# Performance work log

Hardware: AMD Instinct MI355X
Metric: run time of the kernel (lower is better)

## Reference

```python
import jax, jax.numpy as jnp
import numpy as np

B, T, V, D, SLOTS = 16, 4096, 32000, 512, 256
EPS = 1e-5


def setup_inputs() -> dict:
    key = jax.random.key(0)
    ks = jax.random.split(key, 12)
    s = 0.02
    return {
        "seq": jax.random.randint(ks[0], (B, T), 0, V),
        "emb": jax.random.normal(ks[1], (V, D), jnp.float32) * s,
        "w1": jax.random.normal(ks[2], (D, 2 * D), jnp.float32) * s,
        "b1": jnp.zeros((2 * D,), jnp.float32),
        "w2": jax.random.normal(ks[3], (2 * D, D), jnp.float32) * s,
        "b2": jnp.zeros((D,), jnp.float32),
        "ln_g": jnp.ones((D,), jnp.float32),
        "ln_b": jnp.zeros((D,), jnp.float32),
        "wg": jax.random.normal(ks[4], (D,), jnp.float32) * s,
        "bg": jnp.zeros((), jnp.float32),
        "wq": jax.random.normal(ks[5], (D, D), jnp.float32) * s,
        "bq": jnp.zeros((D,), jnp.float32),
        "wo": jax.random.normal(ks[6], (D, V), jnp.float32) * s,
        "bo": jnp.zeros((V,), jnp.float32),
    }


def reference(seq, emb, w1, b1, w2, b2, ln_g, ln_b, wg, bg, wq, bq, wo, bo):
    # Encoder: embed -> residual FFN -> LayerNorm
    h0 = emb[seq]                                        # [B,T,D]
    ff = jax.nn.relu(h0 @ w1 + b1) @ w2 + b2             # [B,T,D]
    x = h0 + ff
    mu = jnp.mean(x, axis=-1, keepdims=True)
    var = jnp.mean(jnp.square(x - mu), axis=-1, keepdims=True)
    h = (x - mu) * jax.lax.rsqrt(var + EPS) * ln_g + ln_b  # [B,T,D]

    # Gate -> top-k slot selection -> gather memory
    gate = jax.nn.sigmoid(h @ wg + bg)                   # [B,T]
    topk = min(SLOTS, T)
    _, top_idx = jax.lax.top_k(gate, topk)               # [B,K]
    memory = jnp.take_along_axis(h, top_idx[:, :, None], axis=1)  # [B,K,D]

    # Single-query masked softmax attention (mask is all ones)
    query_h = h[:, -1, :]                                # [B,D]
    q = query_h @ wq + bq                                # [B,D]
    scores = jnp.einsum('bkd,bd->bk', memory, q)         # [B,K]
    mask = jnp.ones((seq.shape[0], topk), jnp.float32)
    scores = jnp.where(mask == 0, -1e9, scores)
    attn = jax.nn.softmax(scores, axis=-1)               # [B,K]
    ctx = jnp.einsum('bk,bkd->bd', attn, memory)         # [B,D]
    return ctx @ wo + bo                                 # [B,V]
```

## Files before the change

### kernel.cpp

```cpp
#include <hip/hip_runtime.h>

typedef __bf16 bf16x8 __attribute__((ext_vector_type(8)));
typedef float f32x4 __attribute__((ext_vector_type(4)));
typedef unsigned short ushort8v __attribute__((ext_vector_type(8)));

#define NB 16
#define NT 4096
#define NV 32000
#define ND 512
#define NH 1024
#define NSLOTS 256

__device__ __forceinline__ float b2f(unsigned short u) {
  unsigned int x = ((unsigned int)u) << 16;
  return __builtin_bit_cast(float, x);
}
__device__ __forceinline__ unsigned short f2b(float f) {
  unsigned int x = __builtin_bit_cast(unsigned int, f);
  unsigned int r = (x + 0x7FFFu + ((x >> 16) & 1u)) >> 16;
  return (unsigned short)r;
}

#define GLOAD_LDS16(g, l)                                                              \
  __builtin_amdgcn_global_load_lds((const __attribute__((address_space(1))) void*)(g), \
                                   (__attribute__((address_space(3))) void*)(l), 16, 0, 0)
#define BARRIER() asm volatile("s_barrier" ::: "memory")
#define VMCNT(n) asm volatile("s_waitcnt vmcnt(" #n ")" ::: "memory")

__global__ __launch_bounds__(256) void cvtwt_kernel(
    const float* __restrict__ emb, unsigned short* __restrict__ embb,
    const float* __restrict__ w1, const float* __restrict__ w2,
    unsigned short* __restrict__ w1t, unsigned short* __restrict__ w2t) {
  const int blk = blockIdx.x;
  if (blk < 8000) {
    const long base = ((long)blk * 256 + threadIdx.x) * 8;
    float4 a = *(const float4*)&emb[base];
    float4 b = *(const float4*)&emb[base + 4];
    ushort8v o;
    o[0] = f2b(a.x); o[1] = f2b(a.y); o[2] = f2b(a.z); o[3] = f2b(a.w);
    o[4] = f2b(b.x); o[5] = f2b(b.y); o[6] = f2b(b.z); o[7] = f2b(b.w);
    *(ushort8v*)&embb[base] = o;
  } else {
    const int i = (blk - 8000) * 256 + threadIdx.x;
    if (i < ND * NH) {
      const int n = i >> 9, k = i & 511;
      w1t[i] = f2b(w1[k * NH + n]);
    } else {
      const int j = i - ND * NH;
      const int n = j >> 10, k = j & 1023;
      w2t[j] = f2b(w2[k * ND + n]);
    }
  }
}

template <int KDIM, int NLD, int NBN, bool RELU>
__global__ __launch_bounds__(256) void gemm128_kernel(
    const unsigned short* __restrict__ Abase, const unsigned short* __restrict__ Bt,
    const float* __restrict__ bias, unsigned short* __restrict__ Out) {
  __shared__ union {
    unsigned short AB[3][2][128 * 32];
    unsigned short C[128 * 136];
  } sm;
  const int tid = threadIdx.x;
  const int lane = tid & 63;
  const int w = tid >> 6;

  const int id = blockIdx.x;
  const int swz = (id & 7) * (gridDim.x >> 3) + (id >> 3);
  const int bm = swz / NBN;
  const int bn = swz % NBN;

  const int wm = w >> 1, wn = w & 1;

  const int rgrp = lane >> 2;
  const int schunk = (lane & 3) ^ ((lane >> 3) & 3);
  const unsigned short* aptr[2];
  const unsigned short* bptr[2];
#pragma unroll
  for (int r = 0; r < 2; ++r) {
    const int grp = w * 2 + r;
    const int arow = bm * 128 + grp * 16 + rgrp;
    aptr[r] = Abase + (size_t)arow * (size_t)KDIM + schunk * 8;
    const int brow = bn * 128 + grp * 16 + rgrp;
    bptr[r] = Bt + (size_t)brow * (size_t)KDIM + schunk * 8;
  }

  const int fr = lane & 15;
  const int fhi = lane >> 4;
  const int fsw = (fr >> 1) & 3;
  const int fchunk = (fhi ^ fsw) * 8;
  int aoff[4], boff[4];
#pragma unroll
  for (int m = 0; m < 4; ++m) aoff[m] = (wm * 64 + m * 16 + fr) * 32 + fchunk;
#pragma unroll
  for (int n = 0; n < 4; ++n) boff[n] = (wn * 64 + n * 16 + fr) * 32 + fchunk;

  f32x4 acc[4][4] = {};

  auto stage = [&](int buf, int kt) {
#pragma unroll
    for (int r = 0; r < 2; ++r) {
      const int grp = w * 2 + r;
      GLOAD_LDS16(aptr[r] + kt * 32, &sm.AB[buf][0][grp * 512]);
      GLOAD_LDS16(bptr[r] + kt * 32, &sm.AB[buf][1][grp * 512]);
    }
  };

  constexpr int NKT = KDIM / 32;
  stage(0, 0);
  stage(1, 1);
  for (int kt = 0; kt < NKT; ++kt) {
    if (kt + 1 < NKT)
      asm volatile("s_waitcnt vmcnt(4)" ::: "memory");
    else
      asm volatile("s_waitcnt vmcnt(0)" ::: "memory");
    __builtin_amdgcn_s_barrier();
    if (kt + 2 < NKT) stage((kt + 2) % 3, kt + 2);
    const int cur = kt % 3;
    bf16x8 af[4], bfr[4];
#pragma unroll
    for (int m = 0; m < 4; ++m)
      af[m] = __builtin_bit_cast(bf16x8, *(const ushort8v*)&sm.AB[cur][0][aoff[m]]);
#pragma unroll
    for (int n = 0; n < 4; ++n)
      bfr[n] = __builtin_bit_cast(bf16x8, *(const ushort8v*)&sm.AB[cur][1][boff[n]]);
    __builtin_amdgcn_s_setprio(1);
#pragma unroll
    for (int m = 0; m < 4; ++m)
#pragma unroll
      for (int n = 0; n < 4; ++n)
        acc[m][n] = __builtin_amdgcn_mfma_f32_16x16x32_bf16(af[m], bfr[n], acc[m][n], 0, 0, 0);
    __builtin_amdgcn_s_setprio(0);
  }
  __builtin_amdgcn_s_barrier();

#pragma unroll
  for (int m = 0; m < 4; ++m)
#pragma unroll
    for (int n = 0; n < 4; ++n) {
      const int col_l = wn * 64 + n * 16 + fr;
      const float bb = bias[bn * 128 + col_l];
      const int row_l0 = wm * 64 + m * 16 + (fhi << 2);
#pragma unroll
      for (int i = 0; i < 4; ++i) {
        float v = acc[m][n][i] + bb;
        if constexpr (RELU) v = fmaxf(v, 0.f);
        sm.C[(row_l0 + i) * 136 + col_l] = f2b(v);
      }
    }
  __syncthreads();
#pragma unroll
  for (int r8 = 0; r8 < 8; ++r8) {
    const int chunk = r8 * 256 + tid;
    const int row = chunk >> 4;
    const int c8 = (chunk & 15) * 8;
    ushort8v v = *(const ushort8v*)&sm.C[row * 136 + c8];
    *(ushort8v*)&Out[(size_t)(bm * 128 + row) * (size_t)NLD + bn * 128 + c8] = v;
  }
}

__global__ __launch_bounds__(256) void lnv_kernel(
    const float* __restrict__ emb, const unsigned short* __restrict__ FFv,
    unsigned short* __restrict__ Hv, const float* __restrict__ ln_g,
    const float* __restrict__ ln_b, const float* __restrict__ wg,
    const float* __restrict__ bgp, float* __restrict__ gatev,
    const int* __restrict__ seq, float* __restrict__ hlast) {
  const int lane = threadIdx.x & 63;
  const int w = threadIdx.x >> 6;
  const int v = blockIdx.x * 4 + w;
  const float* er = emb + (size_t)v * ND + lane * 8;
  ushort8v fv = *(const ushort8v*)&FFv[(size_t)v * ND + lane * 8];
  float4 e0 = *(const float4*)er, e1 = *(const float4*)(er + 4);
  float x[8] = {b2f(fv[0]) + e0.x, b2f(fv[1]) + e0.y, b2f(fv[2]) + e0.z, b2f(fv[3]) + e0.w,
                b2f(fv[4]) + e1.x, b2f(fv[5]) + e1.y, b2f(fv[6]) + e1.z, b2f(fv[7]) + e1.w};
  float s = 0.f, sq = 0.f;
#pragma unroll
  for (int j = 0; j < 8; ++j) {
    s += x[j];
    sq += x[j] * x[j];
  }
#pragma unroll
  for (int o = 32; o; o >>= 1) {
    s += __shfl_xor(s, o);
    sq += __shfl_xor(sq, o);
  }
  const float mu = s * (1.f / 512.f);
  const float var = sq * (1.f / 512.f) - mu * mu;
  const float rs = rsqrtf(var + 1e-5f);
  float gd = 0.f;
  float h[8];
  ushort8v hv;
#pragma unroll
  for (int j = 0; j < 8; ++j) {
    const int col = lane * 8 + j;
    h[j] = (x[j] - mu) * rs * ln_g[col] + ln_b[col];
    hv[j] = f2b(h[j]);
    gd += h[j] * wg[col];
  }
  *(ushort8v*)&Hv[(size_t)v * ND + lane * 8] = hv;
#pragma unroll
  for (int o = 32; o; o >>= 1) gd += __shfl_xor(gd, o);
  if (lane == 0) gatev[v] = 1.f / (1.f + expf(-(gd + bgp[0])));
  for (int b = 0; b < NB; ++b) {
    if (seq[b * NT + NT - 1] == v) {
      float* hl = hlast + b * ND + lane * 8;
#pragma unroll
      for (int j = 0; j < 8; ++j) hl[j] = h[j];
    }
  }
}

__global__ __launch_bounds__(256) void topk_qpart_kernel(
    const float* __restrict__ gatev, const int* __restrict__ seq,
    int* __restrict__ topidx, const float* __restrict__ hlast,
    const float* __restrict__ wq, const float* __restrict__ bq,
    float* __restrict__ qpart) {
  __shared__ int wsum[2][4];
  __shared__ unsigned int scanbuf[256];
  const int tid = threadIdx.x;
  if (blockIdx.x >= 16) {
    const int blk = blockIdx.x - 16;
    const int b = blk >> 3, s = blk & 7;
    const int d0 = s * 64;
    float a0 = 0.f, a1 = 0.f;
#pragma unroll 4
    for (int dd = 0; dd < 64; ++dd) {
      const float hv = hlast[b * ND + d0 + dd];
      a0 += hv * wq[(size_t)(d0 + dd) * ND + tid];
      a1 += hv * wq[(size_t)(d0 + dd) * ND + tid + 256];
    }
    if (s == 0) {
      a0 += bq[tid];
      a1 += bq[tid + 256];
    }
    float* qp = qpart + ((size_t)b * 8 + s) * ND;
    qp[tid] = a0;
    qp[tid + 256] = a1;
    return;
  }
  const int b = blockIdx.x;
  const int wv = tid >> 6;
  const int lane = tid & 63;
  const int* sq_ = seq + (size_t)b * NT;
  const int base = tid * 16;
  unsigned int kreg[16];
#pragma unroll
  for (int j = 0; j < 16; ++j)
    kreg[j] = __builtin_bit_cast(unsigned int, gatev[sq_[base + j]]);

  unsigned int K = 0u;
  for (int bit = 31; bit >= 0; --bit) {
    const unsigned int cand = K | (1u << bit);
    int c = 0;
#pragma unroll
    for (int j = 0; j < 16; ++j) c += (kreg[j] >= cand) ? 1 : 0;
#pragma unroll
    for (int o = 32; o; o >>= 1) c += __shfl_xor(c, o);
    const int par = bit & 1;
    if (lane == 0) wsum[par][wv] = c;
    __syncthreads();
    const int tot = wsum[par][0] + wsum[par][1] + wsum[par][2] + wsum[par][3];
    if (tot >= NSLOTS) K = cand;
  }
  int gcnt = 0, ecnt = 0;
#pragma unroll
  for (int j = 0; j < 16; ++j) {
    gcnt += (kreg[j] > K) ? 1 : 0;
    ecnt += (kreg[j] == K) ? 1 : 0;
  }
  __syncthreads();
  scanbuf[tid] = ((unsigned int)gcnt << 16) | (unsigned int)ecnt;
  __syncthreads();
  for (int off = 1; off < 256; off <<= 1) {
    unsigned int v2 = (tid >= off) ? scanbuf[tid - off] : 0u;
    __syncthreads();
    scanbuf[tid] += v2;
    __syncthreads();
  }
  const unsigned int my = scanbuf[tid];
  const unsigned int tot = scanbuf[255];
  const int gi = (int)(my >> 16);
  const int ei = (int)(my & 0xFFFFu);
  const int tot_gt = (int)(tot >> 16);
  int gpos = gi - gcnt;
  int epos = tot_gt + (ei - ecnt);
  int* outp = topidx + b * NSLOTS;
#pragma unroll
  for (int j = 0; j < 16; ++j) {
    if (kreg[j] > K) {
      outp[gpos++] = base + j;
    } else if (kreg[j] == K) {
      if (epos < NSLOTS) outp[epos] = base + j;
      epos++;
    }
  }
}

__global__ __launch_bounds__(256) void attn_kernel(
    const unsigned short* __restrict__ Hv, const int* __restrict__ seq,
    const float* __restrict__ qpart, const int* __restrict__ topidx,
    float* __restrict__ ctx) {
  __shared__ float qs[512];
  __shared__ float attnv[256];
  __shared__ int idxs[256];
  __shared__ float red[4];
  __shared__ float part[2][128];
  const int blk = blockIdx.x;
  const int b = blk >> 2, dc = blk & 3;
  const int tid = threadIdx.x;
  const int lane = tid & 63, wv = tid >> 6;
  {
    float a0 = 0.f, a1 = 0.f;
#pragma unroll
    for (int s = 0; s < 8; ++s) {
      const float* qp = qpart + ((size_t)b * 8 + s) * ND;
      a0 += qp[tid];
      a1 += qp[tid + 256];
    }
    qs[tid] = a0;
    qs[tid + 256] = a1;
  }
  idxs[tid] = seq[(size_t)b * NT + topidx[b * 256 + tid]];
  __syncthreads();
  const unsigned short* hr = Hv + (size_t)idxs[tid] * ND;
  float sc = 0.f;
  for (int d0 = 0; d0 < 512; d0 += 8) {
    ushort8v hv = *(const ushort8v*)&hr[d0];
#pragma unroll
    for (int j = 0; j < 8; ++j) sc += b2f(hv[j]) * qs[d0 + j];
  }
  float m = sc;
#pragma unroll
  for (int o = 32; o; o >>= 1) m = fmaxf(m, __shfl_xor(m, o));
  if (lane == 0) red[wv] = m;
  __syncthreads();
  m = fmaxf(fmaxf(red[0], red[1]), fmaxf(red[2], red[3]));
  __syncthreads();
  const float e = expf(sc - m);
  float ssum = e;
#pragma unroll
  for (int o = 32; o; o >>= 1) ssum += __shfl_xor(ssum, o);
  if (lane == 0) red[wv] = ssum;
  __syncthreads();
  ssum = red[0] + red[1] + red[2] + red[3];
  attnv[tid] = e / ssum;
  __syncthreads();
  const int d = dc * 128 + (tid & 127);
  const int kh = tid >> 7;
  float c = 0.f;
#pragma unroll 4
  for (int k2 = 0; k2 < 128; ++k2) {
    const int k = kh * 128 + k2;
    c += attnv[k] * b2f(Hv[(size_t)idxs[k] * ND + d]);
  }
  part[kh][tid & 127] = c;
  __syncthreads();
  if (tid < 128) ctx[b * 512 + dc * 128 + tid] = part[0][tid] + part[1][tid];
}

__global__ __launch_bounds__(256) void out_part_kernel(const float* __restrict__ ctx,
                                                       const float* __restrict__ wo,
                                                       float* __restrict__ part) {
  const int blk = blockIdx.x;
  const int ct = blk % 125, s = blk / 125;
  const int v = ct * 256 + threadIdx.x;
  const int d0 = s * 64;
  const float* wp = wo + (size_t)d0 * NV + v;
  float acc[16] = {};
#pragma unroll 4
  for (int dd = 0; dd < 64; ++dd) {
    const float wv = wp[(size_t)dd * NV];
#pragma unroll
    for (int bb = 0; bb < 16; ++bb) acc[bb] += ctx[bb * ND + d0 + dd] * wv;
  }
  float* pp = part + (size_t)s * NB * NV + v;
#pragma unroll
  for (int bb = 0; bb < 16; ++bb) pp[(size_t)bb * NV] = acc[bb];
}

__global__ __launch_bounds__(256) void out_reduce_kernel(const float* __restrict__ part,
                                                         const float* __restrict__ bo,
                                                         float* __restrict__ out) {
  const int i = blockIdx.x * 256 + threadIdx.x;
  const int b = i / NV;
  const int v = i - b * NV;
  float a = bo[v];
#pragma unroll
  for (int s = 0; s < 8; ++s) a += part[(size_t)s * NB * NV + i];
  out[i] = a;
}

extern "C" void kernel_launch(void* const* d_in, const int* in_sizes, int n_in,
                              void* d_out, int out_size, void* d_ws, size_t ws_size,
                              hipStream_t stream) {
  const int* seq = (const int*)d_in[0];
  const float* emb = (const float*)d_in[1];
  const float* w1 = (const float*)d_in[2];
  const float* b1 = (const float*)d_in[3];
  const float* w2 = (const float*)d_in[4];
  const float* b2 = (const float*)d_in[5];
  const float* ln_g = (const float*)d_in[6];
  const float* ln_b = (const float*)d_in[7];
  const float* wg = (const float*)d_in[8];
  const float* bg = (const float*)d_in[9];
  const float* wq = (const float*)d_in[10];
  const float* bq = (const float*)d_in[11];
  const float* wo = (const float*)d_in[12];
  const float* bo = (const float*)d_in[13];
  float* out = (float*)d_out;

  char* ws = (char*)d_ws;
  unsigned short* A1v = (unsigned short*)ws;
  unsigned short* FFv = (unsigned short*)(ws + ((size_t)64 << 20));
  unsigned short* embb = (unsigned short*)(ws + ((size_t)96 << 20));
  unsigned short* Hv = (unsigned short*)(ws + ((size_t)128 << 20));
  float* part = (float*)(ws + ((size_t)160 << 20));
  unsigned short* w1t = (unsigned short*)(ws + ((size_t)177 << 20));
  unsigned short* w2t = (unsigned short*)(ws + ((size_t)178 << 20));
  char* sb = ws + ((size_t)180 << 20);
  float* gatev = (float*)sb;
  int* topidx = (int*)(sb + 131072);
  float* hlast = (float*)(sb + 131072 + 16384);
  float* ctxbuf = (float*)(sb + 131072 + 16384 + 32768);
  float* qpart = (float*)(sb + 131072 + 16384 + 65536);

  cvtwt_kernel<<<12096, 256, 0, stream>>>(emb, embb, w1, w2, w1t, w2t);
  gemm128_kernel<512, 1024, 8, true>
      <<<2000, 256, 0, stream>>>(embb, w1t, b1, A1v);
  gemm128_kernel<1024, 512, 4, false>
      <<<1000, 256, 0, stream>>>(A1v, w2t, b2, FFv);
  lnv_kernel<<<8000, 256, 0, stream>>>(emb, FFv, Hv, ln_g, ln_b, wg, bg, gatev, seq, hlast);
  topk_qpart_kernel<<<144, 256, 0, stream>>>(gatev, seq, topidx, hlast, wq, bq, qpart);
  attn_kernel<<<64, 256, 0, stream>>>(Hv, seq, qpart, topidx, ctxbuf);
  out_part_kernel<<<1000, 256, 0, stream>>>(ctxbuf, wo, part);
  out_reduce_kernel<<<2000, 256, 0, stream>>>(part, bo, out);
}
```

Measured before the change: 206.3 us.

## Fuse split-K output projection and reduction into one kernel via LDS

Replaces the two-kernel output projection (partial sums written to global memory, then a separate reduce kernel) with one kernel. Each block covers 32 vocab columns, stages ctx in LDS, computes all 8 K-slices in its warps and reduces them in shared memory before adding the bias. This removes the partial-buffer write/read and one launch, at the cost of narrower per-warp loads of wo. The top-k bit search also skips the two high bits, which are always zero for sigmoid outputs in (0,1).

```diff
diff --git a/kernel.cpp b/kernel.cpp
--- a/kernel.cpp
+++ b/kernel.cpp
@@ -24,8 +24,6 @@
 #define GLOAD_LDS16(g, l)                                                              \
   __builtin_amdgcn_global_load_lds((const __attribute__((address_space(1))) void*)(g), \
                                    (__attribute__((address_space(3))) void*)(l), 16, 0, 0)
-#define BARRIER() asm volatile("s_barrier" ::: "memory")
-#define VMCNT(n) asm volatile("s_waitcnt vmcnt(" #n ")" ::: "memory")
 
 __global__ __launch_bounds__(256) void cvtwt_kernel(
     const float* __restrict__ emb, unsigned short* __restrict__ embb,
@@ -249,7 +247,7 @@
     kreg[j] = __builtin_bit_cast(unsigned int, gatev[sq_[base + j]]);
 
   unsigned int K = 0u;
-  for (int bit = 31; bit >= 0; --bit) {
+  for (int bit = 29; bit >= 0; --bit) {
     const unsigned int cand = K | (1u << bit);
     int c = 0;
 #pragma unroll
@@ -358,36 +356,36 @@
   if (tid < 128) ctx[b * 512 + dc * 128 + tid] = part[0][tid] + part[1][tid];
 }
 
-__global__ __launch_bounds__(256) void out_part_kernel(const float* __restrict__ ctx,
-                                                       const float* __restrict__ wo,
-                                                       float* __restrict__ part) {
-  const int blk = blockIdx.x;
-  const int ct = blk % 125, s = blk / 125;
-  const int v = ct * 256 + threadIdx.x;
-  const int d0 = s * 64;
-  const float* wp = wo + (size_t)d0 * NV + v;
+__global__ __launch_bounds__(256) void out_fused_kernel(const float* __restrict__ ctx,
+                                                        const float* __restrict__ wo,
+                                                        const float* __restrict__ bo,
+                                                        float* __restrict__ out) {
+  __shared__ float cs[16 * 512];
+  __shared__ float red[8][16][32];
+  const int tid = threadIdx.x;
+  const int c = tid & 31, g = tid >> 5;
+  const int v0 = blockIdx.x * 32;
+  for (int i = tid; i < 16 * 512; i += 256) cs[i] = ctx[i];
+  __syncthreads();
+  const int d0 = g * 64;
   float acc[16] = {};
+  const float* wp = wo + (size_t)d0 * NV + v0 + c;
 #pragma unroll 4
   for (int dd = 0; dd < 64; ++dd) {
     const float wv = wp[(size_t)dd * NV];
 #pragma unroll
-    for (int bb = 0; bb < 16; ++bb) acc[bb] += ctx[bb * ND + d0 + dd] * wv;
-  }
-  float* pp = part + (size_t)s * NB * NV + v;
-#pragma unroll
-  for (int bb = 0; bb < 16; ++bb) pp[(size_t)bb * NV] = acc[bb];
-}
-
-__global__ __launch_bounds__(256) void out_reduce_kernel(const float* __restrict__ part,
-                                                         const float* __restrict__ bo,
-                                                         float* __restrict__ out) {
-  const int i = blockIdx.x * 256 + threadIdx.x;
-  const int b = i / NV;
-  const int v = i - b * NV;
-  float a = bo[v];
-#pragma unroll
-  for (int s = 0; s < 8; ++s) a += part[(size_t)s * NB * NV + i];
-  out[i] = a;
+    for (int bb = 0; bb < 16; ++bb) acc[bb] += cs[bb * 512 + d0 + dd] * wv;
+  }
+#pragma unroll
+  for (int bb = 0; bb < 16; ++bb) red[g][bb][c] = acc[bb];
+  __syncthreads();
+  for (int i = tid; i < 512; i += 256) {
+    const int bb = i >> 5, cc = i & 31;
+    float a = bo[v0 + cc];
+#pragma unroll
+    for (int gg = 0; gg < 8; ++gg) a += red[gg][bb][cc];
+    out[(size_t)bb * NV + v0 + cc] = a;
+  }
 }
 
 extern "C" void kernel_launch(void* const* d_in, const int* in_sizes, int n_in,
@@ -414,7 +412,6 @@
   unsigned short* FFv = (unsigned short*)(ws + ((size_t)64 << 20));
   unsigned short* embb = (unsigned short*)(ws + ((size_t)96 << 20));
   unsigned short* Hv = (unsigned short*)(ws + ((size_t)128 << 20));
-  float* part = (float*)(ws + ((size_t)160 << 20));
   unsigned short* w1t = (unsigned short*)(ws + ((size_t)177 << 20));
   unsigned short* w2t = (unsigned short*)(ws + ((size_t)178 << 20));
   char* sb = ws + ((size_t)180 << 20);
@@ -432,6 +429,5 @@
   lnv_kernel<<<8000, 256, 0, stream>>>(emb, FFv, Hv, ln_g, ln_b, wg, bg, gatev, seq, hlast);
   topk_qpart_kernel<<<144, 256, 0, stream>>>(gatev, seq, topidx, hlast, wq, bq, qpart);
   attn_kernel<<<64, 256, 0, stream>>>(Hv, seq, qpart, topidx, ctxbuf);
-  out_part_kernel<<<1000, 256, 0, stream>>>(ctxbuf, wo, part);
-  out_reduce_kernel<<<2000, 256, 0, stream>>>(part, bo, out);
-}
+  out_fused_kernel<<<1000, 256, 0, stream>>>(ctxbuf, wo, bo, out);
+}
```

Result: faster. 199.4 us (-3.4%).
